# Optimization experiments

Measured on AMD Instinct MI355X. Metric: run time of the kernel, lower is better.

## Reference

```python
import jax, jax.numpy as jnp
import numpy as np

N = 100000
E = 1600000
IN_FEATS = 128
H_FEATS = 64
BN_EPS = 1e-5


def setup_inputs() -> dict:
    key = jax.random.key(0)
    ks = jax.random.split(key, 8)
    features = jax.random.normal(ks[0], (N, IN_FEATS), dtype=jnp.float32)
    src = jax.random.randint(ks[1], (E,), 0, N, dtype=jnp.int32)
    dst = jax.random.randint(ks[2], (E,), 0, N, dtype=jnp.int32)
    # GraphConv weights (Glorot-ish scale) and biases
    W1 = jax.random.normal(ks[3], (IN_FEATS, H_FEATS), dtype=jnp.float32) / np.sqrt(IN_FEATS)
    b1 = jnp.zeros((H_FEATS,), dtype=jnp.float32)
    W2 = jax.random.normal(ks[4], (H_FEATS, H_FEATS), dtype=jnp.float32) / np.sqrt(H_FEATS)
    b2 = jnp.zeros((H_FEATS,), dtype=jnp.float32)
    gamma1 = jnp.ones((H_FEATS,), dtype=jnp.float32)
    beta1 = jnp.zeros((H_FEATS,), dtype=jnp.float32)
    gamma2 = jnp.ones((H_FEATS,), dtype=jnp.float32)
    beta2 = jnp.zeros((H_FEATS,), dtype=jnp.float32)
    return {"features": features, "W1": W1, "b1": b1, "gamma1": gamma1,
            "beta1": beta1, "W2": W2, "b2": b2, "gamma2": gamma2,
            "beta2": beta2, "src": src, "dst": dst}


def _degrees(src, dst):
    ones = jnp.ones((E,), dtype=jnp.float32)
    deg_out = jax.ops.segment_sum(ones, src, num_segments=N)
    deg_in = jax.ops.segment_sum(ones, dst, num_segments=N)
    # DGL clamps degree to >= 1 to avoid div by zero
    norm_src = jax.lax.rsqrt(jnp.maximum(deg_out, 1.0))  # [N]
    norm_dst = jax.lax.rsqrt(jnp.maximum(deg_in, 1.0))   # [N]
    return norm_src, norm_dst


def _graph_conv(x, W, b, src, dst, norm_src, norm_dst):
    # norm='both': D_out^{-1/2} scaling on src, sum-aggregate, D_in^{-1/2} on dst
    h = x * norm_src[:, None]          # [N, in]
    h = h @ W                          # [N, out] (transform before aggregate)
    msgs = h[src]                      # [E, out] gather
    agg = jax.ops.segment_sum(msgs, dst, num_segments=N)  # [N, out] scatter-add
    out = agg * norm_dst[:, None] + b
    return jax.nn.elu(out)


def _batch_norm(x, gamma, beta):
    mean = jnp.mean(x, axis=0)
    var = jnp.mean(jnp.square(x - mean), axis=0)
    return (x - mean) * jax.lax.rsqrt(var + BN_EPS) * gamma + beta


def reference(features, W1, b1, gamma1, beta1, W2, b2, gamma2, beta2, src, dst):
    # dropout p=0.0 (eval) -> identity
    norm_src, norm_dst = _degrees(src, dst)
    h1 = _graph_conv(features, W1, b1, src, dst, norm_src, norm_dst)
    h1 = _batch_norm(h1, gamma1, beta1)
    h2 = _graph_conv(h1, W2, b2, src, dst, norm_src, norm_dst)
    h2 = _batch_norm(h2, gamma2, beta2)
    return h2
```

## Files before the change

### kernel.cpp

```cpp
#include <hip/hip_runtime.h>
#include <cmath>

#define NFEAT_IN 128
#define NFEAT_H 64
#define BN_EPS 1e-5f
#define SCAP 2560
#define EPB 8192
#define NBMAX 800

typedef unsigned short ushort_t;
typedef unsigned int uint_t;
typedef __attribute__((ext_vector_type(8))) short short8v;
typedef __attribute__((ext_vector_type(4))) float f32x4;

__device__ inline float b2f(ushort_t u) {
    return __uint_as_float(((uint_t)u) << 16);
}

__device__ inline ushort_t f2b(float f) {
    uint_t x = __float_as_uint(f);
    return (ushort_t)((x + 0x7FFFu + ((x >> 16) & 1u)) >> 16);
}


__global__ __launch_bounds__(256) void block_append_kernel(const int* __restrict__ src,
                                                           const int* __restrict__ dst,
                                                           int* __restrict__ deg_s,
                                                           int* __restrict__ curD,
                                                           uint_t* __restrict__ dbuf,
                                                           int E, int NB) {
    __shared__ int lcnt[NBMAX];
    __shared__ int lcur[NBMAX];
    int t = threadIdx.x;
    int e0 = blockIdx.x * EPB;
    int e1 = min(e0 + EPB, E);
    for (int i = t; i < NB; i += 256) lcnt[i] = 0;
    __syncthreads();
    for (int e = e0 + t; e < e1; e += 256)
        atomicAdd(&lcnt[dst[e] >> 7], 1);
    __syncthreads();
    for (int i = t; i < NB; i += 256) {
        int c = lcnt[i];
        lcur[i] = (c > 0) ? atomicAdd(&curD[i * 16], c) : 0;
    }
    __syncthreads();
    for (int e = e0 + t; e < e1; e += 256) {
        int s = src[e], d = dst[e];
        atomicAdd(&deg_s[s], 1);
        int pos = atomicAdd(&lcur[d >> 7], 1);
        if (pos < SCAP) dbuf[(long long)(d >> 7) * SCAP + pos] = ((uint_t)s << 7) | (uint_t)(d & 127);
    }
}

__global__ __launch_bounds__(256) void deg_append_kernel(const int* __restrict__ src,
                                                         const int* __restrict__ dst,
                                                         int* __restrict__ deg_s,
                                                         int* __restrict__ curD,
                                                         uint_t* __restrict__ dbuf, int E) {
    int e = blockIdx.x * 256 + threadIdx.x;
    if (e < E) {
        int s = src[e], d = dst[e];
        atomicAdd(&deg_s[s], 1);
        int pD = atomicAdd(&curD[(d >> 7) * 16], 1);
        if (pD < SCAP) dbuf[(long long)(d >> 7) * SCAP + pD] = ((uint_t)s << 7) | (uint_t)(d & 127);
    }
}

__global__ __launch_bounds__(256) void bucket_hist_kernel(const uint_t* __restrict__ dbuf,
                                                          const int* __restrict__ curD,
                                                          int* __restrict__ deg_d, int N) {
    __shared__ int hist[128];
    int bb = blockIdx.x;
    int t = threadIdx.x;
    if (t < 128) hist[t] = 0;
    __syncthreads();
    int cnt = curD[bb * 16];
    if (cnt > SCAP) cnt = SCAP;
    long long base = (long long)bb * SCAP;
    for (int i = t; i < cnt; i += 256) atomicAdd(&hist[dbuf[base + i] & 127], 1);
    __syncthreads();
    if (t < 128) {
        int node = bb * 128 + t;
        if (node < N) deg_d[node] = hist[t];
    }
}

__global__ __launch_bounds__(256) void norm_scan_kernel(const int* __restrict__ deg_s,
                                                        const int* __restrict__ deg_d,
                                                        float* __restrict__ norm_s,
                                                        float* __restrict__ norm_d,
                                                        int* __restrict__ start,
                                                        int* __restrict__ counter,
                                                        float* __restrict__ stats, int N) {
    int tid = threadIdx.x;
    int i = blockIdx.x * 256 + tid;
    if (blockIdx.x == 0 && tid < 128) stats[tid] = 0.f;
    int lane = tid & 63, w = tid >> 6;
    int ds = 0, dd = 0;
    if (i < N) { ds = deg_s[i]; dd = deg_d[i]; }
    int pd = (dd + 7) & ~7;

    int x = pd;
#pragma unroll
    for (int off = 1; off < 64; off <<= 1) {
        int y = __shfl_up(x, off, 64);
        if (lane >= off) x += y;
    }
    __shared__ int wsum[4];
    __shared__ int blockbase;
    if (lane == 63) wsum[w] = x;
    __syncthreads();
    if (tid == 0)
        blockbase = atomicAdd(counter, wsum[0] + wsum[1] + wsum[2] + wsum[3]);
    __syncthreads();
    int base = blockbase;
    for (int ww = 0; ww < w; ++ww) base += wsum[ww];
    int st = base + x - pd;

    if (i < N) {
        norm_s[i] = rsqrtf((float)(ds > 1 ? ds : 1));
        norm_d[i] = rsqrtf((float)(dd > 1 ? dd : 1));
        start[i] = st;
    }
}

__global__ __launch_bounds__(256) void bucket_scatter_kernel(const uint_t* __restrict__ dbuf,
                                                             const int* __restrict__ curD,
                                                             const int* __restrict__ start,
                                                             int* __restrict__ col, int N) {
    __shared__ int cur[128];
    __shared__ int sst[128];
    int b = blockIdx.x, t = threadIdx.x;
    if (t < 128) {
        cur[t] = 0;
        int node = b * 128 + t;
        sst[t] = (node < N) ? start[node] : 0;
    }
    __syncthreads();
    int cnt = curD[b * 16];
    if (cnt > SCAP) cnt = SCAP;
    long long base = (long long)b * SCAP;
    for (int i = t; i < cnt; i += 256) {
        uint_t p = dbuf[base + i];
        int d0 = (int)(p & 127u);
        int s = (int)(p >> 7);
        int off = atomicAdd(&cur[d0], 1);
        col[sst[d0] + off] = s;
    }
}


__global__ __launch_bounds__(256) void gemm1_mfma(const float* __restrict__ x,
                                                  const float* __restrict__ W,
                                                  const float* __restrict__ norm,
                                                  ushort_t* __restrict__ out, int n) {
    constexpr int K = 128;
    __shared__ ushort_t sWh[64 * K];
    __shared__ ushort_t sWl[64 * K];
    int tid = threadIdx.x;
    for (int i = tid; i < K * 64; i += 256) {
        int k = i >> 6, f = i & 63;
        float v = W[i];
        ushort_t hi = f2b(v);
        ushort_t lo = f2b(v - b2f(hi));
        int idx = f * K + (((k >> 3) ^ (f & 7)) << 3) + (k & 7);
        sWh[idx] = hi;
        sWl[idx] = lo;
    }
    int w = tid >> 6, l = tid & 63, g = l >> 4;
    int rA = blockIdx.x * 64 + w * 16 + (l & 15);
    f32x4 acc[4];
#pragma unroll
    for (int nt = 0; nt < 4; ++nt) acc[nt] = (f32x4){0.f, 0.f, 0.f, 0.f};
    __syncthreads();

#pragma unroll
    for (int ks = 0; ks < K / 32; ++ks) {
        float av[8];
        if (rA < n) {
            const float* px = x + (long long)rA * K + ks * 32 + g * 8;
            float4 p0 = *(const float4*)px;
            float4 p1 = *(const float4*)(px + 4);
            av[0] = p0.x; av[1] = p0.y; av[2] = p0.z; av[3] = p0.w;
            av[4] = p1.x; av[5] = p1.y; av[6] = p1.z; av[7] = p1.w;
        } else {
#pragma unroll
            for (int j = 0; j < 8; ++j) av[j] = 0.f;
        }
        short8v ah, al;
#pragma unroll
        for (int j = 0; j < 8; ++j) {
            ushort_t h = f2b(av[j]);
            ah[j] = (short)h;
            al[j] = (short)f2b(av[j] - b2f(h));
        }
#pragma unroll
        for (int nt = 0; nt < 4; ++nt) {
            int f = nt * 16 + (l & 15);
            int c = (ks * 4 + g) ^ (f & 7);
            short8v bh = *(const short8v*)&sWh[f * K + (c << 3)];
            short8v bl = *(const short8v*)&sWl[f * K + (c << 3)];
            acc[nt] = __builtin_amdgcn_mfma_f32_16x16x32_bf16(ah, bh, acc[nt], 0, 0, 0);
            acc[nt] = __builtin_amdgcn_mfma_f32_16x16x32_bf16(ah, bl, acc[nt], 0, 0, 0);
            acc[nt] = __builtin_amdgcn_mfma_f32_16x16x32_bf16(al, bh, acc[nt], 0, 0, 0);
        }
    }
    int rb = blockIdx.x * 64 + w * 16 + g * 4;
    float nv[4];
#pragma unroll
    for (int j = 0; j < 4; ++j) {
        int r = rb + j;
        nv[j] = (r < n) ? norm[r] : 0.f;
    }
#pragma unroll
    for (int nt = 0; nt < 4; ++nt) {
        int cc = nt * 16 + (l & 15);
#pragma unroll
        for (int j = 0; j < 4; ++j) {
            int r = rb + j;
            if (r < n) out[(long long)r * 64 + cc] = f2b(acc[nt][j] * nv[j]);
        }
    }
}

__global__ __launch_bounds__(256) void gemm2_mfma(const ushort_t* __restrict__ x,
                                                  const float* __restrict__ W,
                                                  const float* __restrict__ coef,
                                                  const float* __restrict__ biasK,
                                                  const float* __restrict__ norm,
                                                  ushort_t* __restrict__ out, int n) {
    constexpr int K = 64;
    __shared__ ushort_t sWh[64 * K];
    __shared__ ushort_t sWl[64 * K];
    int tid = threadIdx.x;
    for (int i = tid; i < K * 64; i += 256) {
        int k = i >> 6, f = i & 63;
        float v = coef[k] * W[i];
        ushort_t hi = f2b(v);
        ushort_t lo = f2b(v - b2f(hi));
        int idx = f * K + (((k >> 3) ^ (f & 7)) << 3) + (k & 7);
        sWh[idx] = hi;
        sWl[idx] = lo;
    }
    int w = tid >> 6, l = tid & 63, g = l >> 4;
    int rA = blockIdx.x * 64 + w * 16 + (l & 15);
    f32x4 acc[4];
#pragma unroll
    for (int nt = 0; nt < 4; ++nt) acc[nt] = (f32x4){0.f, 0.f, 0.f, 0.f};
    __syncthreads();

#pragma unroll
    for (int ks = 0; ks < 2; ++ks) {
        short8v ah;
        if (rA < n) {
            uint4 u = *(const uint4*)(x + (long long)rA * 64 + ks * 32 + g * 8);
            union { uint4 u; short8v s; } cvt;
            cvt.u = u;
            ah = cvt.s;
        } else {
#pragma unroll
            for (int j = 0; j < 8; ++j) ah[j] = 0;
        }
#pragma unroll
        for (int nt = 0; nt < 4; ++nt) {
            int f = nt * 16 + (l & 15);
            int c = (ks * 4 + g) ^ (f & 7);
            short8v bh = *(const short8v*)&sWh[f * K + (c << 3)];
            short8v bl = *(const short8v*)&sWl[f * K + (c << 3)];
            acc[nt] = __builtin_amdgcn_mfma_f32_16x16x32_bf16(ah, bh, acc[nt], 0, 0, 0);
            acc[nt] = __builtin_amdgcn_mfma_f32_16x16x32_bf16(ah, bl, acc[nt], 0, 0, 0);
        }
    }
    int rb = blockIdx.x * 64 + w * 16 + g * 4;
    float nv[4];
#pragma unroll
    for (int j = 0; j < 4; ++j) {
        int r = rb + j;
        nv[j] = (r < n) ? norm[r] : 0.f;
    }
#pragma unroll
    for (int nt = 0; nt < 4; ++nt) {
        int cc = nt * 16 + (l & 15);
        float bk = biasK[cc];
#pragma unroll
        for (int j = 0; j < 4; ++j) {
            int r = rb + j;
            if (r < n) out[(long long)r * 64 + cc] = f2b((acc[nt][j] + bk) * nv[j]);
        }
    }
}

__global__ __launch_bounds__(256) void quant8_kernel(const ushort_t* __restrict__ h,
                                                     uint2* __restrict__ q8,
                                                     float* __restrict__ qs, int N) {
    int tid = threadIdx.x;
    int w = tid >> 6, lane = tid & 63;
    int j = lane & 7;
    int row = blockIdx.x * 32 + w * 8 + (lane >> 3);
    if (row >= N) return;
    uint4 u = ((const uint4*)(h + (long long)row * 64))[j];
    float v[8];
    v[0] = __uint_as_float(u.x << 16);
    v[1] = __uint_as_float(u.x & 0xFFFF0000u);
    v[2] = __uint_as_float(u.y << 16);
    v[3] = __uint_as_float(u.y & 0xFFFF0000u);
    v[4] = __uint_as_float(u.z << 16);
    v[5] = __uint_as_float(u.z & 0xFFFF0000u);
    v[6] = __uint_as_float(u.w << 16);
    v[7] = __uint_as_float(u.w & 0xFFFF0000u);
    float m = 0.f;
#pragma unroll
    for (int i = 0; i < 8; ++i) m = fmaxf(m, fabsf(v[i]));
    m = fmaxf(m, __shfl_xor(m, 1, 64));
    m = fmaxf(m, __shfl_xor(m, 2, 64));
    m = fmaxf(m, __shfl_xor(m, 4, 64));
    float inv = (m > 0.f) ? 127.f / m : 0.f;
    if (j == 0) qs[row] = (m > 0.f) ? m * (1.f / 127.f) : 0.f;
    int q[8];
#pragma unroll
    for (int i = 0; i < 8; ++i) q[i] = __float2int_rn(v[i] * inv);
    uint2 p;
    p.x = (uint_t)(q[0] & 255) | ((uint_t)(q[1] & 255) << 8) |
          ((uint_t)(q[2] & 255) << 16) | ((uint_t)q[3] << 24);
    p.y = (uint_t)(q[4] & 255) | ((uint_t)(q[5] & 255) << 8) |
          ((uint_t)(q[6] & 255) << 16) | ((uint_t)q[7] << 24);
    q8[(long long)row * 8 + j] = p;
}

__device__ inline void acc_i8(float* acc, uint2 u, float sc) {
    acc[0] += sc * (float)(int)(signed char)(u.x);
    acc[1] += sc * (float)(int)(signed char)(u.x >> 8);
    acc[2] += sc * (float)(int)(signed char)(u.x >> 16);
    acc[3] += sc * (float)(int)(signed char)(u.x >> 24);
    acc[4] += sc * (float)(int)(signed char)(u.y);
    acc[5] += sc * (float)(int)(signed char)(u.y >> 8);
    acc[6] += sc * (float)(int)(signed char)(u.y >> 16);
    acc[7] += sc * (float)(int)(signed char)(u.y >> 24);
}

__global__ __launch_bounds__(256) void agg_fused_kernel(const uint2* __restrict__ q8,
                                                        const float* __restrict__ qs,
                                                        const int* __restrict__ start,
                                                        const int* __restrict__ degd,
                                                        const int* __restrict__ col,
                                                        const float* __restrict__ normd,
                                                        const float* __restrict__ bias,
                                                        ushort_t* __restrict__ outp,
                                                        float* __restrict__ stats, int N) {
    int tid = threadIdx.x;
    int w = tid >> 6;
    int lane = tid & 63;
    int g = lane >> 3;
    int j = lane & 7;

    float bb[8];
#pragma unroll
    for (int i = 0; i < 8; ++i) bb[i] = bias[j * 8 + i];

    float sum[8], sq[8];
#pragma unroll
    for (int i = 0; i < 8; ++i) { sum[i] = 0.f; sq[i] = 0.f; }

    for (int node = blockIdx.x * 4 + w; node < N; node += gridDim.x * 4) {
        int s0 = start[node];
        int d = degd[node];
        float acc[8];
#pragma unroll
        for (int i = 0; i < 8; ++i) acc[i] = 0.f;

        int k = 0;
        for (; k + 16 <= d; k += 16) {
            int c0 = col[s0 + k + g];
            int c1 = col[s0 + k + 8 + g];
            uint2 a = q8[(long long)c0 * 8 + j];
            uint2 b = q8[(long long)c1 * 8 + j];
            float sa = qs[c0];
            float sb = qs[c1];
            acc_i8(acc, a, sa);
            acc_i8(acc, b, sb);
        }
        for (; k + 8 <= d; k += 8) {
            int c0 = col[s0 + k + g];
            uint2 a = q8[(long long)c0 * 8 + j];
            float sa = qs[c0];
            acc_i8(acc, a, sa);
        }
        if (k < d) {
            int idx = k + g;
            if (idx < d) {
                int c0 = col[s0 + idx];
                uint2 a = q8[(long long)c0 * 8 + j];
                float sa = qs[c0];
                acc_i8(acc, a, sa);
            }
        }

#pragma unroll
        for (int i = 0; i < 8; ++i) {
            acc[i] += __shfl_xor(acc[i], 8, 64);
            acc[i] += __shfl_xor(acc[i], 16, 64);
            acc[i] += __shfl_xor(acc[i], 32, 64);
        }

        if (g == 0) {
            float nv = normd[node];
            float v[8];
#pragma unroll
            for (int i = 0; i < 8; ++i) {
                float t = acc[i] * nv + bb[i];
                t = t > 0.f ? t : expm1f(t);
                v[i] = t;
                sum[i] += t;
                sq[i] += t * t;
            }
            uint4 p;
            p.x = ((uint_t)f2b(v[1]) << 16) | f2b(v[0]);
            p.y = ((uint_t)f2b(v[3]) << 16) | f2b(v[2]);
            p.z = ((uint_t)f2b(v[5]) << 16) | f2b(v[4]);
            p.w = ((uint_t)f2b(v[7]) << 16) | f2b(v[6]);
            ((uint4*)(outp + (long long)node * 64))[j] = p;
        }
    }

    __shared__ float ssum[4][64];
    __shared__ float ssq[4][64];
    if (g == 0) {
#pragma unroll
        for (int i = 0; i < 8; ++i) {
            ssum[w][j * 8 + i] = sum[i];
            ssq[w][j * 8 + i] = sq[i];
        }
    }
    __syncthreads();
    if (tid < 64) {
        float s = ssum[0][tid] + ssum[1][tid] + ssum[2][tid] + ssum[3][tid];
        float q = ssq[0][tid] + ssq[1][tid] + ssq[2][tid] + ssq[3][tid];
        atomicAdd(&stats[tid], s);
        atomicAdd(&stats[64 + tid], q);
    }
}

__global__ __launch_bounds__(64) void bn_fin2_kernel(float* __restrict__ stats,
                                                     const float* __restrict__ gamma,
                                                     const float* __restrict__ beta,
                                                     const float* __restrict__ W2,
                                                     float* __restrict__ coef,
                                                     float* __restrict__ biasK, float inv_n) {
    int f = threadIdx.x;
    float mean = stats[f] * inv_n;
    float var = stats[64 + f] * inv_n - mean * mean;
    float a = gamma[f] * rsqrtf(var + BN_EPS);
    float cB = beta[f] - mean * a;
    coef[f] = a;
    coef[64 + f] = cB;
    stats[f] = 0.f;
    stats[64 + f] = 0.f;
    __shared__ float scB[64];
    scB[f] = cB;
    __syncthreads();
    float s = 0.f;
    for (int k = 0; k < 64; ++k) s = fmaf(scB[k], W2[k * 64 + f], s);
    biasK[f] = s;
}

__global__ __launch_bounds__(64) void bn_finalize(float* __restrict__ stats,
                                                  const float* __restrict__ gamma,
                                                  const float* __restrict__ beta,
                                                  float* __restrict__ coef, float inv_n) {
    int f = threadIdx.x;
    float mean = stats[f] * inv_n;
    float var = stats[64 + f] * inv_n - mean * mean;
    float a = gamma[f] * rsqrtf(var + BN_EPS);
    coef[f] = a;
    coef[64 + f] = beta[f] - mean * a;
}

__global__ __launch_bounds__(256) void bn_apply_b2f(const uint4* __restrict__ in,
                                                    const float* __restrict__ coef,
                                                    float4* __restrict__ out, long long n4) {
    long long i = (long long)blockIdx.x * 256 + threadIdx.x;
    if (i >= n4) return;
    int k = (int)((i & 7) << 3);
    uint4 u = in[i];
    float4 a, b;
    a.x = __uint_as_float(u.x << 16) * coef[k] + coef[64 + k];
    a.y = __uint_as_float(u.x & 0xFFFF0000u) * coef[k + 1] + coef[64 + k + 1];
    a.z = __uint_as_float(u.y << 16) * coef[k + 2] + coef[64 + k + 2];
    a.w = __uint_as_float(u.y & 0xFFFF0000u) * coef[k + 3] + coef[64 + k + 3];
    b.x = __uint_as_float(u.z << 16) * coef[k + 4] + coef[64 + k + 4];
    b.y = __uint_as_float(u.z & 0xFFFF0000u) * coef[k + 5] + coef[64 + k + 5];
    b.z = __uint_as_float(u.w << 16) * coef[k + 6] + coef[64 + k + 6];
    b.w = __uint_as_float(u.w & 0xFFFF0000u) * coef[k + 7] + coef[64 + k + 7];
    out[i * 2] = a;
    out[i * 2 + 1] = b;
}


extern "C" void kernel_launch(void* const* d_in, const int* in_sizes, int n_in,
                              void* d_out, int out_size, void* d_ws, size_t ws_size,
                              hipStream_t stream) {
    const float* features = (const float*)d_in[0];
    const float* W1 = (const float*)d_in[1];
    const float* b1 = (const float*)d_in[2];
    const float* gamma1 = (const float*)d_in[3];
    const float* beta1 = (const float*)d_in[4];
    const float* W2 = (const float*)d_in[5];
    const float* b2 = (const float*)d_in[6];
    const float* gamma2 = (const float*)d_in[7];
    const float* beta2 = (const float*)d_in[8];
    const int* src = (const int*)d_in[9];
    const int* dst = (const int*)d_in[10];
    int N = in_sizes[0] / NFEAT_IN;
    int E = in_sizes[9];

    float inv_n = 1.0f / (float)N;
    long long tot = (long long)N * 64;
    int eblk256 = (E + 255) / 256;
    int nblk256 = (N + 255) / 256;
    int NB = (N + 127) >> 7;
    int gblk = (N + 63) / 64;
    int qblk = (N + 31) / 32;
    long long n4 = (long long)N * 8;
    int a4blk = (int)((n4 + 255) / 256);

    long long bufcap = (long long)NB * SCAP;
    long long colcap = (long long)E + 8LL * N;
    long long int_total = (16LL * NB + 4 + 3LL * N + bufcap + colcap + 3) & ~3LL;
    long long flt_count = ((2LL * N + 128 + 128 + 64) + 3) & ~3LL;

    int* ip = (int*)d_ws;
    int* curD = ip;
    int* counter = ip + 16LL * NB;
    int* deg_s = ip + 16LL * NB + 4;
    int* deg_d = deg_s + N;
    int* startv = deg_d + N;
    uint_t* dbuf = (uint_t*)(startv + N);
    int* col = (int*)(dbuf + bufcap);
    float* fp = (float*)(ip + int_total);
    float* norm_s = fp;
    float* norm_d = fp + N;
    float* stats = fp + 2LL * N;
    float* coef = stats + 128;
    float* biasK = coef + 128;
    ushort_t* hA = (ushort_t*)(fp + flt_count);
    ushort_t* oB = hA + tot;
    float* qs = (float*)(oB + tot);
    uint2* q8 = (uint2*)(qs + N);

    hipMemsetAsync(curD, 0, sizeof(int) * (16LL * NB + 4 + N), stream);
    if (NB <= NBMAX) {
        int bblk = (E + EPB - 1) / EPB;
        block_append_kernel<<<bblk, 256, 0, stream>>>(src, dst, deg_s, curD, dbuf, E, NB);
    } else {
        deg_append_kernel<<<eblk256, 256, 0, stream>>>(src, dst, deg_s, curD, dbuf, E);
    }
    bucket_hist_kernel<<<NB, 256, 0, stream>>>(dbuf, curD, deg_d, N);
    norm_scan_kernel<<<nblk256, 256, 0, stream>>>(deg_s, deg_d, norm_s, norm_d,
                                                  startv, counter, stats, N);
    bucket_scatter_kernel<<<NB, 256, 0, stream>>>(dbuf, curD, startv, col, N);

    gemm1_mfma<<<gblk, 256, 0, stream>>>(features, W1, norm_s, hA, N);
    quant8_kernel<<<qblk, 256, 0, stream>>>(hA, q8, qs, N);
    agg_fused_kernel<<<2048, 256, 0, stream>>>(q8, qs, startv, deg_d, col, norm_d, b1,
                                               oB, stats, N);
    bn_fin2_kernel<<<1, 64, 0, stream>>>(stats, gamma1, beta1, W2, coef, biasK, inv_n);

    gemm2_mfma<<<gblk, 256, 0, stream>>>(oB, W2, coef, biasK, norm_s, hA, N);
    quant8_kernel<<<qblk, 256, 0, stream>>>(hA, q8, qs, N);
    agg_fused_kernel<<<2048, 256, 0, stream>>>(q8, qs, startv, deg_d, col, norm_d, b2,
                                               oB, stats, N);
    bn_finalize<<<1, 64, 0, stream>>>(stats, gamma2, beta2, coef, inv_n);
    bn_apply_b2f<<<a4blk, 256, 0, stream>>>((const uint4*)oB, coef, (float4*)d_out, n4);
}
```

Before: 404.1 us.

## Pad CSR rows to multiples of 8 and interleave four nodes per wave in aggregation

The bucket scatter now pads each node's column list up to a multiple of 8 with a sentinel index N, and a zero row is added to the int8 feature table so padded entries contribute nothing. The aggregation kernel processes four nodes per wavefront at once, issuing their gathers together to raise memory-level parallelism and drop the tail-handling branches. This costs more registers, extra gathers of the zero row, and some lanes idling when the four nodes have very different degrees.

```diff
diff --git a/kernel.cpp b/kernel.cpp
--- a/kernel.cpp
+++ b/kernel.cpp
@@ -146,6 +146,16 @@
         int s = (int)(p >> 7);
         int off = atomicAdd(&cur[d0], 1);
         col[sst[d0] + off] = s;
+    }
+    __syncthreads();
+    if (t < 128) {
+        int node = b * 128 + t;
+        if (node < N) {
+            int st = sst[t];
+            int end = st + cur[t];
+            int pend = st + ((cur[t] + 7) & ~7);
+            for (int p = end; p < pend; ++p) col[p] = N;
+        }
     }
 }
 
@@ -297,7 +307,12 @@
     int w = tid >> 6, lane = tid & 63;
     int j = lane & 7;
     int row = blockIdx.x * 32 + w * 8 + (lane >> 3);
-    if (row >= N) return;
+    if (row > N) return;
+    if (row == N) {
+        q8[(long long)row * 8 + j] = make_uint2(0u, 0u);
+        if (j == 0) qs[row] = 0.f;
+        return;
+    }
     uint4 u = ((const uint4*)(h + (long long)row * 64))[j];
     float v[8];
     v[0] = __uint_as_float(u.x << 16);
@@ -361,64 +376,71 @@
 #pragma unroll
     for (int i = 0; i < 8; ++i) { sum[i] = 0.f; sq[i] = 0.f; }
 
-    for (int node = blockIdx.x * 4 + w; node < N; node += gridDim.x * 4) {
-        int s0 = start[node];
-        int d = degd[node];
-        float acc[8];
-#pragma unroll
-        for (int i = 0; i < 8; ++i) acc[i] = 0.f;
-
-        int k = 0;
-        for (; k + 16 <= d; k += 16) {
-            int c0 = col[s0 + k + g];
-            int c1 = col[s0 + k + 8 + g];
-            uint2 a = q8[(long long)c0 * 8 + j];
-            uint2 b = q8[(long long)c1 * 8 + j];
-            float sa = qs[c0];
-            float sb = qs[c1];
-            acc_i8(acc, a, sa);
-            acc_i8(acc, b, sb);
-        }
-        for (; k + 8 <= d; k += 8) {
-            int c0 = col[s0 + k + g];
-            uint2 a = q8[(long long)c0 * 8 + j];
-            float sa = qs[c0];
-            acc_i8(acc, a, sa);
-        }
-        if (k < d) {
-            int idx = k + g;
-            if (idx < d) {
-                int c0 = col[s0 + idx];
-                uint2 a = q8[(long long)c0 * 8 + j];
-                float sa = qs[c0];
-                acc_i8(acc, a, sa);
+    int stride = gridDim.x * 4;
+    for (int base = blockIdx.x * 4 + w; base < N; base += 4 * stride) {
+        int s0[4], pd[4], nd[4];
+#pragma unroll
+        for (int q = 0; q < 4; ++q) {
+            int n = base + q * stride;
+            nd[q] = n;
+            if (n < N) {
+                s0[q] = start[n];
+                pd[q] = (degd[n] + 7) & ~7;
+            } else {
+                s0[q] = 0;
+                pd[q] = 0;
             }
         }
-
-#pragma unroll
-        for (int i = 0; i < 8; ++i) {
-            acc[i] += __shfl_xor(acc[i], 8, 64);
-            acc[i] += __shfl_xor(acc[i], 16, 64);
-            acc[i] += __shfl_xor(acc[i], 32, 64);
-        }
-
-        if (g == 0) {
-            float nv = normd[node];
-            float v[8];
+        int pdmax = max(max(pd[0], pd[1]), max(pd[2], pd[3]));
+
+        float acc[4][8];
+#pragma unroll
+        for (int q = 0; q < 4; ++q)
+#pragma unroll
+            for (int i = 0; i < 8; ++i) acc[q][i] = 0.f;
+
+        for (int k = 0; k < pdmax; k += 8) {
+            int c[4];
+#pragma unroll
+            for (int q = 0; q < 4; ++q)
+                c[q] = (k < pd[q]) ? col[s0[q] + k + g] : -1;
+#pragma unroll
+            for (int q = 0; q < 4; ++q) {
+                if (c[q] >= 0) {
+                    uint2 u = q8[(long long)c[q] * 8 + j];
+                    float sc = qs[c[q]];
+                    acc_i8(acc[q], u, sc);
+                }
+            }
+        }
+
+#pragma unroll
+        for (int q = 0; q < 4; ++q) {
+            if (nd[q] >= N) continue;
 #pragma unroll
             for (int i = 0; i < 8; ++i) {
-                float t = acc[i] * nv + bb[i];
-                t = t > 0.f ? t : expm1f(t);
-                v[i] = t;
-                sum[i] += t;
-                sq[i] += t * t;
+                acc[q][i] += __shfl_xor(acc[q][i], 8, 64);
+                acc[q][i] += __shfl_xor(acc[q][i], 16, 64);
+                acc[q][i] += __shfl_xor(acc[q][i], 32, 64);
             }
-            uint4 p;
-            p.x = ((uint_t)f2b(v[1]) << 16) | f2b(v[0]);
-            p.y = ((uint_t)f2b(v[3]) << 16) | f2b(v[2]);
-            p.z = ((uint_t)f2b(v[5]) << 16) | f2b(v[4]);
-            p.w = ((uint_t)f2b(v[7]) << 16) | f2b(v[6]);
-            ((uint4*)(outp + (long long)node * 64))[j] = p;
+            if (g == 0) {
+                float nv = normd[nd[q]];
+                float v[8];
+#pragma unroll
+                for (int i = 0; i < 8; ++i) {
+                    float t = acc[q][i] * nv + bb[i];
+                    t = t > 0.f ? t : expm1f(t);
+                    v[i] = t;
+                    sum[i] += t;
+                    sq[i] += t * t;
+                }
+                uint4 p;
+                p.x = ((uint_t)f2b(v[1]) << 16) | f2b(v[0]);
+                p.y = ((uint_t)f2b(v[3]) << 16) | f2b(v[2]);
+                p.z = ((uint_t)f2b(v[5]) << 16) | f2b(v[4]);
+                p.w = ((uint_t)f2b(v[7]) << 16) | f2b(v[6]);
+                ((uint4*)(outp + (long long)nd[q] * 64))[j] = p;
+            }
         }
     }
 
@@ -519,7 +541,7 @@
     int nblk256 = (N + 255) / 256;
     int NB = (N + 127) >> 7;
     int gblk = (N + 63) / 64;
-    int qblk = (N + 31) / 32;
+    int qblk = (N + 1 + 31) / 32;
     long long n4 = (long long)N * 8;
     int a4blk = (int)((n4 + 255) / 256);
 
@@ -545,7 +567,7 @@
     ushort_t* hA = (ushort_t*)(fp + flt_count);
     ushort_t* oB = hA + tot;
     float* qs = (float*)(oB + tot);
-    uint2* q8 = (uint2*)(qs + N);
+    uint2* q8 = (uint2*)(qs + N + 4);
 
     hipMemsetAsync(curD, 0, sizeof(int) * (16LL * NB + 4 + N), stream);
     if (NB <= NBMAX) {
```

New measurement: 411.1 us. About the same (+1.7%).

## Partition neighbor lists by source range and aggregate layer one in cooperative phased passes

Applied to the files above, without the earlier changes.

The CSR build now sorts each destination's neighbors into four source-index quarters and records per-quarter counts. A new cooperative kernel with 512 persistent blocks holds per-block node accumulators in LDS. It processes one source quarter at a time with grid syncs between passes, so the gathered int8 feature rows stay in cache (L2 or the MI355X's large last-level cache). This adds an extra pass over the edge buffer in the scatter kernel, four grid-wide barriers, and fewer resident waves, which may cut latency hiding. Only layer one uses it, and the older kernel remains as a fallback.

```diff
diff --git a/kernel.cpp b/kernel.cpp
--- a/kernel.cpp
+++ b/kernel.cpp
@@ -1,5 +1,8 @@
 #include <hip/hip_runtime.h>
+#include <hip/hip_cooperative_groups.h>
 #include <cmath>
+
+namespace cg = cooperative_groups;
 
 #define NFEAT_IN 128
 #define NFEAT_H 64
@@ -124,28 +127,49 @@
     }
 }
 
-__global__ __launch_bounds__(256) void bucket_scatter_kernel(const uint_t* __restrict__ dbuf,
-                                                             const int* __restrict__ curD,
-                                                             const int* __restrict__ start,
-                                                             int* __restrict__ col, int N) {
-    __shared__ int cur[128];
-    __shared__ int sst[128];
+__global__ __launch_bounds__(256) void bucket_scatter2_kernel(const uint_t* __restrict__ dbuf,
+                                                              const int* __restrict__ curD,
+                                                              const int* __restrict__ start,
+                                                              int* __restrict__ col,
+                                                              uint2* __restrict__ rcnt,
+                                                              int N, int Q) {
+    __shared__ int cnt4[128][4];
+    __shared__ int cur[128][4];
     int b = blockIdx.x, t = threadIdx.x;
-    if (t < 128) {
-        cur[t] = 0;
-        int node = b * 128 + t;
-        sst[t] = (node < N) ? start[node] : 0;
-    }
+    if (t < 128) { cnt4[t][0] = 0; cnt4[t][1] = 0; cnt4[t][2] = 0; cnt4[t][3] = 0; }
     __syncthreads();
     int cnt = curD[b * 16];
     if (cnt > SCAP) cnt = SCAP;
     long long base = (long long)b * SCAP;
+    int Q2 = 2 * Q, Q3 = 3 * Q;
     for (int i = t; i < cnt; i += 256) {
         uint_t p = dbuf[base + i];
         int d0 = (int)(p & 127u);
         int s = (int)(p >> 7);
-        int off = atomicAdd(&cur[d0], 1);
-        col[sst[d0] + off] = s;
+        int r = (s >= Q) + (s >= Q2) + (s >= Q3);
+        atomicAdd(&cnt4[d0][r], 1);
+    }
+    __syncthreads();
+    if (t < 128) {
+        int node = b * 128 + t;
+        int st = (node < N) ? start[node] : 0;
+        int c0 = cnt4[t][0], c1 = cnt4[t][1], c2 = cnt4[t][2], c3 = cnt4[t][3];
+        cur[t][0] = st;
+        cur[t][1] = st + c0;
+        cur[t][2] = st + c0 + c1;
+        cur[t][3] = st + c0 + c1 + c2;
+        if (node < N)
+            rcnt[node] = make_uint2((uint_t)c0 | ((uint_t)c1 << 16),
+                                    (uint_t)c2 | ((uint_t)c3 << 16));
+    }
+    __syncthreads();
+    for (int i = t; i < cnt; i += 256) {
+        uint_t p = dbuf[base + i];
+        int d0 = (int)(p & 127u);
+        int s = (int)(p >> 7);
+        int r = (s >= Q) + (s >= Q2) + (s >= Q3);
+        int off = atomicAdd(&cur[d0][r], 1);
+        col[off] = s;
     }
 }
 
@@ -338,6 +362,89 @@
     acc[7] += sc * (float)(int)(signed char)(u.y >> 24);
 }
 
+__global__ __launch_bounds__(512) void coop_agg_kernel(const uint2* __restrict__ q8,
+                                                       const float* __restrict__ qs,
+                                                       const int* __restrict__ start,
+                                                       const uint2* __restrict__ rcnt,
+                                                       const int* __restrict__ col,
+                                                       const float* __restrict__ normd,
+                                                       const float* __restrict__ bias,
+                                                       ushort_t* __restrict__ outp,
+                                                       float* __restrict__ stats,
+                                                       int N, int npb) {
+    extern __shared__ float sacc[];
+    cg::grid_group grid = cg::this_grid();
+    int tid = threadIdx.x;
+    int w = tid >> 6, lane = tid & 63;
+    int g = lane >> 3, j = lane & 7;
+    int base = blockIdx.x * npb;
+
+    int totf = npb * 64;
+    for (int i = tid; i < totf; i += 512) sacc[i] = 0.f;
+    __syncthreads();
+
+    for (int r = 0; r < 4; ++r) {
+        for (int l = w; l < npb; l += 8) {
+            int gn = base + l;
+            if (gn < N) {
+                uint2 rc = rcnt[gn];
+                int c0 = (int)(rc.x & 0xFFFFu), c1 = (int)(rc.x >> 16);
+                int c2 = (int)(rc.y & 0xFFFFu), c3 = (int)(rc.y >> 16);
+                int pre, cnt;
+                if (r == 0) { pre = 0; cnt = c0; }
+                else if (r == 1) { pre = c0; cnt = c1; }
+                else if (r == 2) { pre = c0 + c1; cnt = c2; }
+                else { pre = c0 + c1 + c2; cnt = c3; }
+                if (cnt > 0) {
+                    int s0 = start[gn] + pre;
+                    float a8[8];
+#pragma unroll
+                    for (int i = 0; i < 8; ++i) a8[i] = 0.f;
+                    for (int k = g; k < cnt; k += 8) {
+                        int c = col[s0 + k];
+                        uint2 u = q8[(long long)c * 8 + j];
+                        float sc = qs[c];
+                        acc_i8(a8, u, sc);
+                    }
+#pragma unroll
+                    for (int i = 0; i < 8; ++i) {
+                        a8[i] += __shfl_xor(a8[i], 8, 64);
+                        a8[i] += __shfl_xor(a8[i], 16, 64);
+                        a8[i] += __shfl_xor(a8[i], 32, 64);
+                    }
+                    if (g == 0) {
+#pragma unroll
+                        for (int i = 0; i < 8; ++i) sacc[l * 64 + j * 8 + i] += a8[i];
+                    }
+                }
+            }
+        }
+        grid.sync();
+    }
+
+    float b = bias[lane];
+    float sum = 0.f, sq = 0.f;
+    for (int l = w; l < npb; l += 8) {
+        int gn = base + l;
+        if (gn >= N) continue;
+        float v = sacc[l * 64 + lane] * normd[gn] + b;
+        v = v > 0.f ? v : expm1f(v);
+        outp[(long long)gn * 64 + lane] = f2b(v);
+        sum += v;
+        sq += v * v;
+    }
+    __shared__ float ssum[8][64], ssq[8][64];
+    ssum[w][lane] = sum;
+    ssq[w][lane] = sq;
+    __syncthreads();
+    if (tid < 64) {
+        float s = 0.f, q = 0.f;
+        for (int ww = 0; ww < 8; ++ww) { s += ssum[ww][tid]; q += ssq[ww][tid]; }
+        atomicAdd(&stats[tid], s);
+        atomicAdd(&stats[64 + tid], q);
+    }
+}
+
 __global__ __launch_bounds__(256) void agg_fused_kernel(const uint2* __restrict__ q8,
                                                         const float* __restrict__ qs,
                                                         const int* __restrict__ start,
@@ -520,12 +627,17 @@
     int NB = (N + 127) >> 7;
     int gblk = (N + 63) / 64;
     int qblk = (N + 31) / 32;
+    int Q = (N + 3) / 4;
     long long n4 = (long long)N * 8;
     int a4blk = (int)((n4 + 255) / 256);
 
+    int npb = (N + 511) / 512;
+    size_t ldsB = (size_t)npb * 64 * 4;
+    bool useCoop = (npb <= 220);
+
     long long bufcap = (long long)NB * SCAP;
     long long colcap = (long long)E + 8LL * N;
-    long long int_total = (16LL * NB + 4 + 3LL * N + bufcap + colcap + 3) & ~3LL;
+    long long int_total = (16LL * NB + 4 + 5LL * N + bufcap + colcap + 3) & ~3LL;
     long long flt_count = ((2LL * N + 128 + 128 + 64) + 3) & ~3LL;
 
     int* ip = (int*)d_ws;
@@ -534,7 +646,8 @@
     int* deg_s = ip + 16LL * NB + 4;
     int* deg_d = deg_s + N;
     int* startv = deg_d + N;
-    uint_t* dbuf = (uint_t*)(startv + N);
+    uint2* rcnt = (uint2*)(startv + N);
+    uint_t* dbuf = (uint_t*)(startv + N + 2LL * N);
     int* col = (int*)(dbuf + bufcap);
     float* fp = (float*)(ip + int_total);
     float* norm_s = fp;
@@ -545,7 +658,7 @@
     ushort_t* hA = (ushort_t*)(fp + flt_count);
     ushort_t* oB = hA + tot;
     float* qs = (float*)(oB + tot);
-    uint2* q8 = (uint2*)(qs + N);
+    uint2* q8 = (uint2*)(qs + ((N + 3) & ~3));
 
     hipMemsetAsync(curD, 0, sizeof(int) * (16LL * NB + 4 + N), stream);
     if (NB <= NBMAX) {
@@ -557,12 +670,29 @@
     bucket_hist_kernel<<<NB, 256, 0, stream>>>(dbuf, curD, deg_d, N);
     norm_scan_kernel<<<nblk256, 256, 0, stream>>>(deg_s, deg_d, norm_s, norm_d,
                                                   startv, counter, stats, N);
-    bucket_scatter_kernel<<<NB, 256, 0, stream>>>(dbuf, curD, startv, col, N);
+    bucket_scatter2_kernel<<<NB, 256, 0, stream>>>(dbuf, curD, startv, col, rcnt, N, Q);
 
     gemm1_mfma<<<gblk, 256, 0, stream>>>(features, W1, norm_s, hA, N);
     quant8_kernel<<<qblk, 256, 0, stream>>>(hA, q8, qs, N);
-    agg_fused_kernel<<<2048, 256, 0, stream>>>(q8, qs, startv, deg_d, col, norm_d, b1,
-                                               oB, stats, N);
+    if (useCoop) {
+        const uint2* q8c = q8;
+        const float* qsc = qs;
+        const int* stc = startv;
+        const uint2* rcc = rcnt;
+        const int* colc = col;
+        const float* ndc = norm_d;
+        const float* b1c = b1;
+        ushort_t* oBc = oB;
+        float* stsc = stats;
+        void* kargs[] = {(void*)&q8c, (void*)&qsc, (void*)&stc, (void*)&rcc, (void*)&colc,
+                         (void*)&ndc, (void*)&b1c, (void*)&oBc, (void*)&stsc,
+                         (void*)&N, (void*)&npb};
+        hipLaunchCooperativeKernel((void*)coop_agg_kernel, dim3(512), dim3(512),
+                                   kargs, (unsigned int)ldsB, stream);
+    } else {
+        agg_fused_kernel<<<2048, 256, 0, stream>>>(q8, qs, startv, deg_d, col, norm_d, b1,
+                                                   oB, stats, N);
+    }
     bn_fin2_kernel<<<1, 64, 0, stream>>>(stats, gamma1, beta1, W2, coef, biasK, inv_n);
 
     gemm2_mfma<<<gblk, 256, 0, stream>>>(oB, W2, coef, biasK, norm_s, hA, N);
```

After: 724.1 us. +79.2%, slower.
